# Optimization experiments

Measured on AMD Instinct MI355X. Metric: run time of the kernel, lower is better.

The kernel has to match this reference:

```python
import jax, jax.numpy as jnp
import numpy as np

IN_SIZE, R = 80, 5
D = 256  # hidden size used throughout
OUT = IN_SIZE * R  # 400


def gru_cell(x, h, Wih, Whh, bih, bhh):
    # torch.nn.GRUCell semantics
    gi = x @ Wih.T + bih
    gh = h @ Whh.T + bhh
    ir, iz, in_ = jnp.split(gi, 3, axis=-1)
    hr, hz, hn = jnp.split(gh, 3, axis=-1)
    r = jax.nn.sigmoid(ir + hr)
    z = jax.nn.sigmoid(iz + hz)
    n = jnp.tanh(in_ + r * hn)
    return (1.0 - z) * n + z * h


def setup_inputs() -> dict:
    key = jax.random.key(0)
    ks = jax.random.split(key, 32)
    s = 0.05
    inp = {
        'encoder_outputs': jax.random.normal(ks[0], (128, 512, D), jnp.float32),
        'inputs': jax.random.normal(ks[1], (128, 1000, IN_SIZE), jnp.float32),
        # Prenet: Linear(400,256), Linear(256,128)
        'W1': jax.random.normal(ks[2], (256, OUT)) * s, 'b1': jnp.zeros((256,)),
        'W2': jax.random.normal(ks[3], (128, 256)) * s, 'b2': jnp.zeros((128,)),
        # attn GRUCell(384 -> 256)
        'Wih_a': jax.random.normal(ks[4], (3 * D, 128 + D)) * s,
        'Whh_a': jax.random.normal(ks[5], (3 * D, D)) * s,
        'bih_a': jnp.zeros((3 * D,)), 'bhh_a': jnp.zeros((3 * D,)),
        # Bahdanau attention: query_layer (no bias) and v: Linear(256,1,no bias)
        'Wq': jax.random.normal(ks[6], (D, D)) * s,
        'v': jax.random.normal(ks[7], (D,)) * s,
        # memory_layer Linear(256,256,no bias)
        'Wm': jax.random.normal(ks[8], (D, D)) * s,
        # pre_rnn_dec_proj Linear(512,256)
        'Wp': jax.random.normal(ks[9], (D, 2 * D)) * s, 'bp': jnp.zeros((D,)),
        # two decoder GRUCells(256 -> 256)
        'Wih_d1': jax.random.normal(ks[10], (3 * D, D)) * s,
        'Whh_d1': jax.random.normal(ks[11], (3 * D, D)) * s,
        'bih_d1': jnp.zeros((3 * D,)), 'bhh_d1': jnp.zeros((3 * D,)),
        'Wih_d2': jax.random.normal(ks[12], (3 * D, D)) * s,
        'Whh_d2': jax.random.normal(ks[13], (3 * D, D)) * s,
        'bih_d2': jnp.zeros((3 * D,)), 'bhh_d2': jnp.zeros((3 * D,)),
        # mel projection Linear(256, 400)
        'Wmel': jax.random.normal(ks[14], (OUT, D)) * s, 'bmel': jnp.zeros((OUT,)),
    }
    return inp


def reference(encoder_outputs, inputs, W1, b1, W2, b2,
              Wih_a, Whh_a, bih_a, bhh_a, Wq, v, Wm, Wp, bp,
              Wih_d1, Whh_d1, bih_d1, bhh_d1,
              Wih_d2, Whh_d2, bih_d2, bhh_d2, Wmel, bmel):
    B = encoder_outputs.shape[0]
    processed_mem = encoder_outputs @ Wm.T               # (B, T_enc, D)
    # teacher forcing: (B, T_mel, in_size) -> (T_dec, B, in_size*r)
    x = inputs.reshape(B, inputs.shape[1] // R, -1).transpose(1, 0, 2)
    # decoder input at step t is frame t-1 (zeros at t=0)
    x_shift = jnp.concatenate([jnp.zeros_like(x[:1]), x[:-1]], axis=0)

    def step(carry, x_t):
        attn_h, h1, h2, ctx = carry
        # prenet (dropout disabled: eval-mode reference)
        pre = jax.nn.relu(x_t @ W1.T + b1)
        pre = jax.nn.relu(pre @ W2.T + b2)                # (B, 128)
        cell_in = jnp.concatenate([pre, ctx], axis=-1)    # (B, 384)
        attn_h = gru_cell(cell_in, attn_h, Wih_a, Whh_a, bih_a, bhh_a)
        q = attn_h @ Wq.T                                 # (B, D)
        logits = jnp.tanh(q[:, None, :] + processed_mem) @ v  # (B, T_enc)
        align = jax.nn.softmax(logits, axis=-1)
        ctx = jnp.einsum('bt,btd->bd', align, encoder_outputs)
        dec_in = jnp.concatenate([attn_h, ctx], axis=-1) @ Wp.T + bp
        h1 = gru_cell(dec_in, h1, Wih_d1, Whh_d1, bih_d1, bhh_d1)
        dec_in = h1 + dec_in
        h2 = gru_cell(dec_in, h2, Wih_d2, Whh_d2, bih_d2, bhh_d2)
        dec_in = h2 + dec_in
        out = dec_in @ Wmel.T + bmel                      # (B, 400)
        return (attn_h, h1, h2, ctx), (out, align)

    z = jnp.zeros((B, D), encoder_outputs.dtype)
    init = (z, z, z, z)
    _, (outs, aligns) = jax.lax.scan(step, init, x_shift)
    outputs = outs.transpose(1, 0, 2)       # (B, T_dec, 400)
    alignments = aligns.transpose(1, 0, 2)  # (B, T_dec, T_enc)
    return outputs, alignments
```

## Files before the change

### kernel.cpp

```cpp
#include <hip/hip_runtime.h>

typedef _Float16 h2f __attribute__((ext_vector_type(2)));

#define LOG2E 1.44269504088896f

__device__ __forceinline__ float fexp2(float x){ return __builtin_amdgcn_exp2f(x); }
__device__ __forceinline__ float frcp (float x){ return __builtin_amdgcn_rcpf(x); }
__device__ __forceinline__ float sigm (float x){ return frcp(1.f + fexp2(-LOG2E*x)); }
__device__ __forceinline__ float tanhf2(float x){
  x = fminf(15.f, fmaxf(-15.f, x));
  float e = fexp2(2.f*LOG2E*x);
  return (e-1.f)*frcp(e+1.f);
}
__device__ __forceinline__ unsigned pkh2(float a, float b){
  h2f h; h.x = (_Float16)a; h.y = (_Float16)b;
  return __builtin_bit_cast(unsigned, h);
}

#if __has_builtin(__builtin_amdgcn_fdot2)
__device__ __forceinline__ float dot2(unsigned a, unsigned b, float c){
  return __builtin_amdgcn_fdot2(__builtin_bit_cast(h2f,a), __builtin_bit_cast(h2f,b), c, false);
}
#else
__device__ __forceinline__ float dot2(unsigned a, unsigned b, float c){
  h2f ha=__builtin_bit_cast(h2f,a), hb=__builtin_bit_cast(h2f,b);
  return c + (float)ha.x*(float)hb.x + (float)ha.y*(float)hb.y;
}
#endif

__device__ __forceinline__ void dot8_2(uint4 w, uint4 x, float& a0, float& a1){
  a0 = dot2(w.x, x.x, a0); a1 = dot2(w.y, x.y, a1);
  a0 = dot2(w.z, x.z, a0); a1 = dot2(w.w, x.w, a1);
}

template<int N, int K8>
__device__ __forceinline__ float mv(const uint4* __restrict__ W, const uint4* __restrict__ xs, int n){
  float a0 = 0.f, a1 = 0.f;
  #pragma unroll 4
  for (int k8 = 0; k8 < K8; ++k8)
    dot8_2(W[k8*N + n], xs[k8], a0, a1);
  return a0 + a1;
}

template<int N, int K8, int C>
__device__ __forceinline__ float mvc(const uint4* __restrict__ W, const uint4* __restrict__ xs, int n){
  float a0 = 0.f, a1 = 0.f;
  int k8 = 0;
  #pragma unroll 1
  for (; k8 + C <= K8; k8 += C){
    uint4 w[C];
    #pragma unroll
    for (int i = 0; i < C; ++i) w[i] = W[(size_t)(k8+i)*N + n];
    #pragma unroll
    for (int i = 0; i < C; ++i) dot8_2(w[i], xs[k8+i], a0, a1);
  }
  if constexpr (K8 % C){
    constexpr int R = K8 % C;
    uint4 w[R];
    #pragma unroll
    for (int i = 0; i < R; ++i) w[i] = W[(size_t)(k8+i)*N + n];
    #pragma unroll
    for (int i = 0; i < R; ++i) dot8_2(w[i], xs[k8+i], a0, a1);
  }
  return a0 + a1;
}

static constexpr size_t OFF_W1   = 0;
static constexpr size_t OFF_W2   = 204800;
static constexpr size_t OFF_WIHA = 270336;
static constexpr size_t OFF_WHHA = 860160;
static constexpr size_t OFF_WQ   = 1253376;
static constexpr size_t OFF_WP   = 1384448;
static constexpr size_t OFF_WD1I = 1646592;
static constexpr size_t OFF_WD1H = 2039808;
static constexpr size_t OFF_WD2I = 2433024;
static constexpr size_t OFF_WD2H = 2826240;
static constexpr size_t OFF_WMEL = 3219456;
static constexpr size_t OFF_WM   = 3424256;
static constexpr size_t OFF_TPM  = 3555328;
static constexpr size_t OFF_ENCH = 37109760;

__global__ void pack_w(const float* __restrict__ src, uint4* __restrict__ dst, int N, int K8){
  int idx = blockIdx.x*blockDim.x + threadIdx.x;
  if (idx >= N*K8) return;
  int n = idx % N, k8 = idx / N;
  const float* s = src + (size_t)n*(K8*8) + k8*8;
  dst[idx] = make_uint4(pkh2(s[0],s[1]), pkh2(s[2],s[3]), pkh2(s[4],s[5]), pkh2(s[6],s[7]));
}

__global__ void conv_enc(const float* __restrict__ enc, unsigned* __restrict__ encH){
  size_t i = blockIdx.x*(size_t)blockDim.x + threadIdx.x;
  if (i >= (size_t)128*512*128) return;
  const float2 f = *(const float2*)(enc + 2*i);
  encH[i] = pkh2(f.x, f.y);
}

__global__ __launch_bounds__(1024) void pm_kernel(const float* __restrict__ enc,
    const uint4* __restrict__ Wmp, unsigned* __restrict__ tpm)
{
  int b = blockIdx.y, tc = blockIdx.x;
  int tid = threadIdx.x;
  __shared__ __align__(16) unsigned s_e[4][128];
  if (tid < 512){
    int r = tid >> 7, d2 = tid & 127;
    const float2 f = *(const float2*)(enc + ((size_t)b*512 + tc*4 + r)*256 + 2*d2);
    s_e[r][d2] = pkh2(f.x, f.y);
  }
  __syncthreads();
  int d = tid & 255, r = tid >> 8;
  float acc = mv<256,32>(Wmp, (const uint4*)s_e[r], d);
  float tq = tanhf2(acc);
  float hi = __shfl_down(tq, 1);
  if ((d & 1) == 0)
    tpm[(size_t)b*65536 + (size_t)(d>>1)*512 + (tc*4 + r)] = pkh2(tq, hi);
}

__global__ __launch_bounds__(256) void prenet_kernel(
    const float* __restrict__ inputs,
    const float* __restrict__ b1, const float* __restrict__ b2,
    const uint4* __restrict__ W1p, const uint4* __restrict__ W2p,
    float* __restrict__ out)
{
  int t = blockIdx.x, b = blockIdx.y;
  int tid = threadIdx.x;
  __shared__ __align__(16) unsigned s_x[200];
  __shared__ __align__(16) unsigned s_p1[128];
  __shared__ float s_a[256];
  if (tid < 200){
    unsigned xv = 0u;
    if (t > 0){
      const float2 f = *(const float2*)(inputs + (size_t)b*80000 + (size_t)(t-1)*400 + 2*tid);
      xv = pkh2(f.x, f.y);
    }
    s_x[tid] = xv;
  }
  __syncthreads();
  float a = fmaxf(mv<256,50>(W1p, (const uint4*)s_x, tid) + b1[tid], 0.f);
  s_a[tid] = a;
  __syncthreads();
  if (tid < 128) s_p1[tid] = pkh2(s_a[2*tid], s_a[2*tid+1]);
  __syncthreads();
  if (tid < 128){
    float p = fmaxf(mv<128,32>(W2p, (const uint4*)s_p1, tid) + b2[tid], 0.f);
    float pN = __shfl_down(p, 1);
    if (!(tid & 1)){
      unsigned* dst = (unsigned*)(out + (size_t)10240000 + ((size_t)b*200 + t)*512);
      dst[tid>>1] = pkh2(p, pN);
    }
  }
}

__global__ __launch_bounds__(512) void mel_kernel(
    const float* __restrict__ bmel, const uint4* __restrict__ Wmelp,
    float* __restrict__ out)
{
  int t = blockIdx.x, b = blockIdx.y;
  int tid = threadIdx.x;
  __shared__ __align__(16) unsigned s_d[128];
  float* po = out + ((size_t)b*200 + t)*400;
  if (tid < 128) s_d[tid] = ((const unsigned*)po)[tid];
  __syncthreads();
  if (tid < 400){
    float r = mvc<400,32,8>(Wmelp, (const uint4*)s_d, tid) + bmel[tid];
    __builtin_nontemporal_store(r, &po[tid]);
  }
}

__global__ __launch_bounds__(1024, 1) void decoder(
   const float* __restrict__ biha, const float* __restrict__ bhha,
   const float* __restrict__ vvec, const float* __restrict__ bp,
   const float* __restrict__ bd1i, const float* __restrict__ bd1h,
   const float* __restrict__ bd2i, const float* __restrict__ bd2h,
   const uint4* __restrict__ Wihap, const uint4* __restrict__ Whhap,
   const uint4* __restrict__ Wqp, const uint4* __restrict__ Wpp,
   const uint4* __restrict__ Wd1ip, const uint4* __restrict__ Wd1hp,
   const uint4* __restrict__ Wd2ip, const uint4* __restrict__ Wd2hp,
   const unsigned* __restrict__ tpm, const unsigned* __restrict__ encH,
   float* __restrict__ out)
{
  const int tid = threadIdx.x;
  const int b = blockIdx.x;

  __shared__ __align__(16) unsigned s_cin2[192];
  __shared__ __align__(16) unsigned s_cat2[256];
  __shared__ __align__(16) unsigned s_di2[128];
  __shared__ __align__(16) unsigned s_h12[128];
  __shared__ __align__(16) unsigned s_h22[128];
  __shared__ float  s_gha[768], s_gh1[768], s_gh2[768];
  __shared__ float  s_g[768];
  __shared__ float  s_ahf[256], s_h1f[256], s_h2f[256];
  __shared__ float  s_dif[256];
  __shared__ float4 s_tv[128];
  __shared__ float  s_lp[2][512];
  __shared__ float2 s_cp[8][128];
  __shared__ float  s_mvp[4][256];
  __shared__ float  s_align[512];
  __shared__ float  s_red[16];

  if (tid < 192) s_cin2[tid] = 0u;
  if (tid < 256){ s_cat2[tid]=0u; s_ahf[tid]=0.f; s_h1f[tid]=0.f; s_h2f[tid]=0.f; }
  if (tid < 128){ s_h12[tid]=0u; s_h22[tid]=0u;
                  s_tv[tid].z = vvec[2*tid]; s_tv[tid].w = vvec[2*tid+1]; }
  __syncthreads();

  const unsigned* tpmB = tpm  + (size_t)b*65536;
  const unsigned* encB = encH + (size_t)b*65536;
  float* outMel = out + (size_t)b*200*400;
  float* outAl  = out + (size_t)10240000 + (size_t)b*200*512;

  for (int t = 0; t < 200; ++t){
    if (tid < 768){
      s_gha[tid] = mvc<768,32,8>(Whhap, (const uint4*)s_cat2, tid) + bhha[tid];
    } else if (tid < 960){
      int r = tid - 768;
      s_gh2[r] = mvc<768,32,8>(Wd2hp, (const uint4*)s_h22, r) + bd2h[r];
    } else {
      s_cin2[tid-960] = ((const unsigned*)(outAl + (size_t)t*512))[tid-960];
    }
    __syncthreads();
    if (tid < 768){
      s_gh1[tid] = mvc<768,32,8>(Wd1hp, (const uint4*)s_h12, tid) + bd1h[tid];
    } else {
      int r = 192 + tid - 768;
      s_gh2[r] = mvc<768,32,8>(Wd2hp, (const uint4*)s_h22, r) + bd2h[r];
    }
    __syncthreads();
    if (tid < 768){
      float gi = mvc<768,48,8>(Wihap, (const uint4*)s_cin2, tid) + biha[tid];
      s_g[tid] = (tid < 512) ? sigm(gi + s_gha[tid]) : gi;
    } else {
      int r = 448 + tid - 768;
      s_gh2[r] = mvc<768,32,8>(Wd2hp, (const uint4*)s_h22, r) + bd2h[r];
    }
    __syncthreads();
    if (tid < 256){
      float rr = s_g[tid], z = s_g[256+tid];
      float nv = tanhf2(s_g[512+tid] + rr*s_gha[512+tid]);
      float h  = nv + z*(s_ahf[tid] - nv);
      s_ahf[tid] = h;
      float hN = __shfl_down(h, 1);
      if (!(tid&1)) s_cat2[tid>>1] = pkh2(h, hN);
    } else if (tid < 320){
      int r = 704 + tid - 256;
      s_gh2[r] = mvc<768,32,8>(Wd2hp, (const uint4*)s_h22, r) + bd2h[r];
    }
    __syncthreads();
    if (tid < 512){
      int n = tid & 255, p = tid >> 8;
      s_mvp[p][n] = mvc<256,16,8>(Wqp + (size_t)p*16*256, (const uint4*)s_cat2 + p*16, n);
    }
    __syncthreads();
    if (tid < 256){
      float q = s_mvp[0][tid] + s_mvp[1][tid];
      ((float*)&s_tv[tid>>1])[tid&1] = tanhf2(q);
    }
    __syncthreads();
    {
      int tt = tid & 511, dh = tid >> 9;
      const unsigned* tp = tpmB + tt + (size_t)dh*32768;
      float acc = 0.f;
      #pragma unroll 1
      for (int c = 0; c < 64; c += 16){
        unsigned tw[16];
        #pragma unroll
        for (int i = 0; i < 16; ++i) tw[i] = __builtin_nontemporal_load(&tp[(size_t)(c+i)*512]);
        #pragma unroll
        for (int i = 0; i < 16; ++i){
          h2f ta = __builtin_bit_cast(h2f, tw[i]);
          float4 tv = s_tv[dh*64 + c + i];
          float ta0 = (float)ta.x, ta1 = (float)ta.y;
          acc += tv.z*(ta0+tv.x)*frcp(1.f+ta0*tv.x)
               + tv.w*(ta1+tv.y)*frcp(1.f+ta1*tv.y);
        }
      }
      s_lp[dh][tt] = acc;
    }
    __syncthreads();
    float ee = 0.f;
    if (tid < 512){
      float lg = s_lp[0][tid] + s_lp[1][tid];
      ee = fexp2(LOG2E*lg);
      float s = ee;
      #pragma unroll
      for (int off = 32; off >= 1; off >>= 1) s += __shfl_xor(s, off);
      if ((tid & 63) == 0) s_red[tid>>6] = s;
    }
    __syncthreads();
    if (tid < 512){
      float S = (s_red[0]+s_red[1])+(s_red[2]+s_red[3])
              + (s_red[4]+s_red[5])+(s_red[6]+s_red[7]);
      float a = ee * frcp(S);
      s_align[tid] = a;
      __builtin_nontemporal_store(a, &outAl[(size_t)t*512 + tid]);
    }
    __syncthreads();
    {
      int d2 = tid & 127, tc = tid >> 7;
      const unsigned* eb = encB + d2 + (size_t)tc*8192;
      float ax = 0.f, ay = 0.f;
      #pragma unroll 1
      for (int c = 0; c < 64; c += 16){
        unsigned ew[16];
        #pragma unroll
        for (int i = 0; i < 16; ++i) ew[i] = __builtin_nontemporal_load(&eb[(size_t)(c+i)*128]);
        #pragma unroll
        for (int i = 0; i < 16; ++i){
          float a = s_align[tc*64 + c + i];
          h2f e2 = __builtin_bit_cast(h2f, ew[i]);
          ax += a*(float)e2.x; ay += a*(float)e2.y;
        }
      }
      s_cp[tc][d2] = make_float2(ax, ay);
    }
    __syncthreads();
    if (tid < 256){
      const float* cp = (const float*)s_cp;
      float c = 0.f;
      #pragma unroll
      for (int k = 0; k < 8; ++k) c += cp[k*256 + tid];
      float cN = __shfl_down(c, 1);
      if (!(tid&1)){ unsigned pk = pkh2(c, cN); s_cin2[64+(tid>>1)] = pk; s_cat2[128+(tid>>1)] = pk; }
    }
    __syncthreads();
    {
      int n = tid & 255, p = tid >> 8;
      s_mvp[p][n] = mvc<256,16,8>(Wpp + (size_t)p*16*256, (const uint4*)s_cat2 + p*16, n);
    }
    __syncthreads();
    if (tid < 256){
      float di = s_mvp[0][tid]+s_mvp[1][tid]+s_mvp[2][tid]+s_mvp[3][tid] + bp[tid];
      s_dif[tid] = di;
      float dN = __shfl_down(di, 1);
      if (!(tid&1)) s_di2[tid>>1] = pkh2(di, dN);
    }
    __syncthreads();
    if (tid < 768){
      float gi = mvc<768,32,8>(Wd1ip, (const uint4*)s_di2, tid) + bd1i[tid];
      s_g[tid] = (tid < 512) ? sigm(gi + s_gh1[tid]) : gi;
    }
    __syncthreads();
    if (tid < 256){
      float rr = s_g[tid], z = s_g[256+tid];
      float nv = tanhf2(s_g[512+tid] + rr*s_gh1[512+tid]);
      float h  = nv + z*(s_h1f[tid] - nv);
      s_h1f[tid] = h;
      float di = s_dif[tid] + h; s_dif[tid] = di;
      float hN = __shfl_down(h, 1), dN = __shfl_down(di, 1);
      if (!(tid&1)){ s_h12[tid>>1] = pkh2(h, hN); s_di2[tid>>1] = pkh2(di, dN); }
    }
    __syncthreads();
    if (tid < 768){
      float gi = mvc<768,32,8>(Wd2ip, (const uint4*)s_di2, tid) + bd2i[tid];
      s_g[tid] = (tid < 512) ? sigm(gi + s_gh2[tid]) : gi;
    }
    __syncthreads();
    if (tid < 256){
      float rr = s_g[tid], z = s_g[256+tid];
      float nv = tanhf2(s_g[512+tid] + rr*s_gh2[512+tid]);
      float h  = nv + z*(s_h2f[tid] - nv);
      s_h2f[tid] = h;
      float di = s_dif[tid] + h;
      float hN = __shfl_down(h, 1), dN = __shfl_down(di, 1);
      if (!(tid&1)){
        unsigned dpk = pkh2(di, dN);
        s_h22[tid>>1] = pkh2(h, hN);
        s_di2[tid>>1] = dpk;
        ((unsigned*)(outMel + (size_t)t*400))[tid>>1] = dpk;
      }
    }
    __syncthreads();
  }
}

extern "C" void kernel_launch(void* const* d_in, const int* in_sizes, int n_in,
                              void* d_out, int out_size, void* d_ws, size_t ws_size,
                              hipStream_t stream){
  (void)in_sizes; (void)n_in; (void)out_size; (void)ws_size;
  const float* enc    = (const float*)d_in[0];
  const float* inputs = (const float*)d_in[1];
  const float* W1 = (const float*)d_in[2];   const float* b1 = (const float*)d_in[3];
  const float* W2 = (const float*)d_in[4];   const float* b2 = (const float*)d_in[5];
  const float* Wiha = (const float*)d_in[6]; const float* Whha = (const float*)d_in[7];
  const float* biha = (const float*)d_in[8]; const float* bhha = (const float*)d_in[9];
  const float* Wq = (const float*)d_in[10];  const float* v  = (const float*)d_in[11];
  const float* Wm = (const float*)d_in[12];
  const float* Wp = (const float*)d_in[13];  const float* bp = (const float*)d_in[14];
  const float* Wd1i = (const float*)d_in[15]; const float* Wd1h = (const float*)d_in[16];
  const float* bd1i = (const float*)d_in[17]; const float* bd1h = (const float*)d_in[18];
  const float* Wd2i = (const float*)d_in[19]; const float* Wd2h = (const float*)d_in[20];
  const float* bd2i = (const float*)d_in[21]; const float* bd2h = (const float*)d_in[22];
  const float* Wmel = (const float*)d_in[23]; const float* bmel = (const float*)d_in[24];

  char* ws = (char*)d_ws;
  uint4* W1p   = (uint4*)(ws + OFF_W1);
  uint4* W2p   = (uint4*)(ws + OFF_W2);
  uint4* Wihap = (uint4*)(ws + OFF_WIHA);
  uint4* Whhap = (uint4*)(ws + OFF_WHHA);
  uint4* Wqp   = (uint4*)(ws + OFF_WQ);
  uint4* Wpp   = (uint4*)(ws + OFF_WP);
  uint4* Wd1ip = (uint4*)(ws + OFF_WD1I);
  uint4* Wd1hp = (uint4*)(ws + OFF_WD1H);
  uint4* Wd2ip = (uint4*)(ws + OFF_WD2I);
  uint4* Wd2hp = (uint4*)(ws + OFF_WD2H);
  uint4* Wmelp = (uint4*)(ws + OFF_WMEL);
  uint4* Wmp   = (uint4*)(ws + OFF_WM);
  unsigned* tpm  = (unsigned*)(ws + OFF_TPM);
  unsigned* encH = (unsigned*)(ws + OFF_ENCH);

  auto P = [&](const float* s, uint4* dst, int N, int K){
    int k8 = K/8, tot = N*k8;
    pack_w<<<(tot+255)/256, 256, 0, stream>>>(s, dst, N, k8);
  };
  P(W1, W1p, 256, 400);   P(W2, W2p, 128, 256);
  P(Wiha, Wihap, 768, 384); P(Whha, Whhap, 768, 256);
  P(Wq, Wqp, 256, 256);   P(Wm, Wmp, 256, 256);
  P(Wp, Wpp, 256, 512);
  P(Wd1i, Wd1ip, 768, 256); P(Wd1h, Wd1hp, 768, 256);
  P(Wd2i, Wd2ip, 768, 256); P(Wd2h, Wd2hp, 768, 256);
  P(Wmel, Wmelp, 400, 256);

  conv_enc<<<32768, 256, 0, stream>>>(enc, encH);
  pm_kernel<<<dim3(128,128), 1024, 0, stream>>>(enc, Wmp, tpm);
  prenet_kernel<<<dim3(200,128), 256, 0, stream>>>(inputs, b1, b2, W1p, W2p, (float*)d_out);

  decoder<<<128, 1024, 0, stream>>>(
      biha, bhha, v, bp, bd1i, bd1h, bd2i, bd2h,
      Wihap, Whhap, Wqp, Wpp, Wd1ip, Wd1hp, Wd2ip, Wd2hp,
      tpm, encH, (float*)d_out);

  mel_kernel<<<dim3(200,128), 512, 0, stream>>>(bmel, Wmelp, (float*)d_out);
}
```

Baseline: 8.842 ms.

## Process two batch elements per decoder block to reuse weight loads

Measured after the change: 12.90 ms. 45.9% more time.

```diff
diff --git a/kernel.cpp b/kernel.cpp
--- a/kernel.cpp
+++ b/kernel.cpp
@@ -45,24 +45,34 @@
 template<int N, int K8, int C>
 __device__ __forceinline__ float mvc(const uint4* __restrict__ W, const uint4* __restrict__ xs, int n){
   float a0 = 0.f, a1 = 0.f;
-  int k8 = 0;
   #pragma unroll 1
-  for (; k8 + C <= K8; k8 += C){
+  for (int k8 = 0; k8 + C <= K8; k8 += C){
     uint4 w[C];
     #pragma unroll
     for (int i = 0; i < C; ++i) w[i] = W[(size_t)(k8+i)*N + n];
     #pragma unroll
     for (int i = 0; i < C; ++i) dot8_2(w[i], xs[k8+i], a0, a1);
   }
-  if constexpr (K8 % C){
-    constexpr int R = K8 % C;
-    uint4 w[R];
+  return a0 + a1;
+}
+
+template<int N, int K8, int C>
+__device__ __forceinline__ void mvc2(const uint4* __restrict__ W,
+    const uint4* __restrict__ xs0, const uint4* __restrict__ xs1, int n,
+    float& o0, float& o1){
+  float a0=0.f, b0=0.f, a1=0.f, b1=0.f;
+  #pragma unroll 1
+  for (int k8 = 0; k8 < K8; k8 += C){
+    uint4 w[C];
     #pragma unroll
-    for (int i = 0; i < R; ++i) w[i] = W[(size_t)(k8+i)*N + n];
+    for (int i = 0; i < C; ++i) w[i] = W[(size_t)(k8+i)*N + n];
     #pragma unroll
-    for (int i = 0; i < R; ++i) dot8_2(w[i], xs[k8+i], a0, a1);
-  }
-  return a0 + a1;
+    for (int i = 0; i < C; ++i){
+      dot8_2(w[i], xs0[k8+i], a0, b0);
+      dot8_2(w[i], xs1[k8+i], a1, b1);
+    }
+  }
+  o0 = a0 + b0; o1 = a1 + b1;
 }
 
 static constexpr size_t OFF_W1   = 0;
@@ -111,8 +121,10 @@
   float acc = mv<256,32>(Wmp, (const uint4*)s_e[r], d);
   float tq = tanhf2(acc);
   float hi = __shfl_down(tq, 1);
-  if ((d & 1) == 0)
-    tpm[(size_t)b*65536 + (size_t)(d>>1)*512 + (tc*4 + r)] = pkh2(tq, hi);
+  if ((d & 1) == 0){
+    int t = tc*4 + r;
+    tpm[ (((size_t)b*32 + (d>>3))*512 + t)*4 + ((d>>1)&3) ] = pkh2(tq, hi);
+  }
 }
 
 __global__ __launch_bounds__(256) void prenet_kernel(
@@ -179,193 +191,240 @@
    float* __restrict__ out)
 {
   const int tid = threadIdx.x;
-  const int b = blockIdx.x;
-
-  __shared__ __align__(16) unsigned s_cin2[192];
-  __shared__ __align__(16) unsigned s_cat2[256];
-  __shared__ __align__(16) unsigned s_di2[128];
-  __shared__ __align__(16) unsigned s_h12[128];
-  __shared__ __align__(16) unsigned s_h22[128];
-  __shared__ float  s_gha[768], s_gh1[768], s_gh2[768];
-  __shared__ float  s_g[768];
-  __shared__ float  s_ahf[256], s_h1f[256], s_h2f[256];
-  __shared__ float  s_dif[256];
-  __shared__ float4 s_tv[128];
+  const int b0 = 2*blockIdx.x, b1v = b0 + 1;
+
+  __shared__ __align__(16) unsigned s_cin2[2][192];
+  __shared__ __align__(16) unsigned s_cat2[2][256];
+  __shared__ __align__(16) unsigned s_di2[2][128];
+  __shared__ __align__(16) unsigned s_h12[2][128];
+  __shared__ __align__(16) unsigned s_h22[2][128];
+  __shared__ float  s_gha[2][768], s_gh1[2][768], s_gh2[2][768];
+  __shared__ float  s_g[2][768];
+  __shared__ float  s_ahf[2][256], s_h1f[2][256], s_h2f[2][256];
+  __shared__ float  s_dif[2][256];
+  __shared__ float4 s_tv[2][128];
   __shared__ float  s_lp[2][512];
-  __shared__ float2 s_cp[8][128];
-  __shared__ float  s_mvp[4][256];
-  __shared__ float  s_align[512];
-  __shared__ float  s_red[16];
-
-  if (tid < 192) s_cin2[tid] = 0u;
-  if (tid < 256){ s_cat2[tid]=0u; s_ahf[tid]=0.f; s_h1f[tid]=0.f; s_h2f[tid]=0.f; }
-  if (tid < 128){ s_h12[tid]=0u; s_h22[tid]=0u;
-                  s_tv[tid].z = vvec[2*tid]; s_tv[tid].w = vvec[2*tid+1]; }
-  __syncthreads();
-
-  const unsigned* tpmB = tpm  + (size_t)b*65536;
-  const unsigned* encB = encH + (size_t)b*65536;
-  float* outMel = out + (size_t)b*200*400;
-  float* outAl  = out + (size_t)10240000 + (size_t)b*200*512;
+  __shared__ float2 s_cp[2][16][32][4];
+  __shared__ float  s_mvp[2][4][256];
+  __shared__ float  s_align[2][512];
+  __shared__ float  s_red[2][8];
+
+  if (tid < 384){ int be=tid/192, i=tid%192; s_cin2[be][i] = 0u; }
+  if (tid < 512){ int be=tid>>8, i=tid&255;
+    s_cat2[be][i]=0u; s_ahf[be][i]=0.f; s_h1f[be][i]=0.f; s_h2f[be][i]=0.f; }
+  if (tid < 256){ int be=tid>>7, i=tid&127;
+    s_h12[be][i]=0u; s_h22[be][i]=0u;
+    s_tv[be][i].z = vvec[2*i]; s_tv[be][i].w = vvec[2*i+1]; }
+  __syncthreads();
+
+  const unsigned* encB[2] = { encH + (size_t)b0*65536, encH + (size_t)b1v*65536 };
+  const uint4*    tpm4[2] = { (const uint4*)tpm + (size_t)b0*16384,
+                              (const uint4*)tpm + (size_t)b1v*16384 };
+  float* outMel[2] = { out + (size_t)b0*80000, out + (size_t)b1v*80000 };
+  float* outAl [2] = { out + 10240000ull + (size_t)b0*102400,
+                       out + 10240000ull + (size_t)b1v*102400 };
+
+  const uint4* cin4[2] = { (const uint4*)s_cin2[0], (const uint4*)s_cin2[1] };
+  const uint4* cat4[2] = { (const uint4*)s_cat2[0], (const uint4*)s_cat2[1] };
+  const uint4* di4 [2] = { (const uint4*)s_di2[0],  (const uint4*)s_di2[1]  };
+  const uint4* h14 [2] = { (const uint4*)s_h12[0],  (const uint4*)s_h12[1]  };
+  const uint4* h24 [2] = { (const uint4*)s_h22[0],  (const uint4*)s_h22[1]  };
 
   for (int t = 0; t < 200; ++t){
     if (tid < 768){
-      s_gha[tid] = mvc<768,32,8>(Whhap, (const uint4*)s_cat2, tid) + bhha[tid];
+      float o0,o1; mvc2<768,32,8>(Whhap, cat4[0], cat4[1], tid, o0, o1);
+      s_gha[0][tid] = o0 + bhha[tid]; s_gha[1][tid] = o1 + bhha[tid];
     } else if (tid < 960){
       int r = tid - 768;
-      s_gh2[r] = mvc<768,32,8>(Wd2hp, (const uint4*)s_h22, r) + bd2h[r];
+      float o0,o1; mvc2<768,32,8>(Wd2hp, h24[0], h24[1], r, o0, o1);
+      s_gh2[0][r] = o0 + bd2h[r]; s_gh2[1][r] = o1 + bd2h[r];
     } else {
-      s_cin2[tid-960] = ((const unsigned*)(outAl + (size_t)t*512))[tid-960];
+      int j = tid - 960;
+      s_cin2[0][j] = ((const unsigned*)(outAl[0] + (size_t)t*512))[j];
+      s_cin2[1][j] = ((const unsigned*)(outAl[1] + (size_t)t*512))[j];
     }
     __syncthreads();
     if (tid < 768){
-      s_gh1[tid] = mvc<768,32,8>(Wd1hp, (const uint4*)s_h12, tid) + bd1h[tid];
+      float o0,o1; mvc2<768,32,8>(Wd1hp, h14[0], h14[1], tid, o0, o1);
+      s_gh1[0][tid] = o0 + bd1h[tid]; s_gh1[1][tid] = o1 + bd1h[tid];
     } else {
       int r = 192 + tid - 768;
-      s_gh2[r] = mvc<768,32,8>(Wd2hp, (const uint4*)s_h22, r) + bd2h[r];
+      float o0,o1; mvc2<768,32,8>(Wd2hp, h24[0], h24[1], r, o0, o1);
+      s_gh2[0][r] = o0 + bd2h[r]; s_gh2[1][r] = o1 + bd2h[r];
     }
     __syncthreads();
     if (tid < 768){
-      float gi = mvc<768,48,8>(Wihap, (const uint4*)s_cin2, tid) + biha[tid];
-      s_g[tid] = (tid < 512) ? sigm(gi + s_gha[tid]) : gi;
+      float o0,o1; mvc2<768,48,8>(Wihap, cin4[0], cin4[1], tid, o0, o1);
+      o0 += biha[tid]; o1 += biha[tid];
+      if (tid < 512){ s_g[0][tid] = sigm(o0 + s_gha[0][tid]); s_g[1][tid] = sigm(o1 + s_gha[1][tid]); }
+      else          { s_g[0][tid] = o0;                        s_g[1][tid] = o1; }
     } else {
       int r = 448 + tid - 768;
-      s_gh2[r] = mvc<768,32,8>(Wd2hp, (const uint4*)s_h22, r) + bd2h[r];
-    }
-    __syncthreads();
-    if (tid < 256){
-      float rr = s_g[tid], z = s_g[256+tid];
-      float nv = tanhf2(s_g[512+tid] + rr*s_gha[512+tid]);
-      float h  = nv + z*(s_ahf[tid] - nv);
-      s_ahf[tid] = h;
+      float o0,o1; mvc2<768,32,8>(Wd2hp, h24[0], h24[1], r, o0, o1);
+      s_gh2[0][r] = o0 + bd2h[r]; s_gh2[1][r] = o1 + bd2h[r];
+    }
+    __syncthreads();
+    if (tid < 512){
+      int be = tid>>8, i = tid&255;
+      float rr = s_g[be][i], z = s_g[be][256+i];
+      float nv = tanhf2(s_g[be][512+i] + rr*s_gha[be][512+i]);
+      float h  = nv + z*(s_ahf[be][i] - nv);
+      s_ahf[be][i] = h;
       float hN = __shfl_down(h, 1);
-      if (!(tid&1)) s_cat2[tid>>1] = pkh2(h, hN);
-    } else if (tid < 320){
-      int r = 704 + tid - 256;
-      s_gh2[r] = mvc<768,32,8>(Wd2hp, (const uint4*)s_h22, r) + bd2h[r];
-    }
-    __syncthreads();
-    if (tid < 512){
-      int n = tid & 255, p = tid >> 8;
-      s_mvp[p][n] = mvc<256,16,8>(Wqp + (size_t)p*16*256, (const uint4*)s_cat2 + p*16, n);
-    }
-    __syncthreads();
-    if (tid < 256){
-      float q = s_mvp[0][tid] + s_mvp[1][tid];
-      ((float*)&s_tv[tid>>1])[tid&1] = tanhf2(q);
-    }
-    __syncthreads();
-    {
-      int tt = tid & 511, dh = tid >> 9;
-      const unsigned* tp = tpmB + tt + (size_t)dh*32768;
+      if (!(i&1)) s_cat2[be][i>>1] = pkh2(h, hN);
+    } else if (tid < 576){
+      int r = 704 + tid - 512;
+      float o0,o1; mvc2<768,32,8>(Wd2hp, h24[0], h24[1], r, o0, o1);
+      s_gh2[0][r] = o0 + bd2h[r]; s_gh2[1][r] = o1 + bd2h[r];
+    }
+    __syncthreads();
+    {
+      int n = tid & 255, p = (tid>>8)&3;
+      float o0,o1; mvc2<256,8,8>(Wqp + (size_t)p*8*256, cat4[0]+p*8, cat4[1]+p*8, n, o0, o1);
+      s_mvp[0][p][n] = o0; s_mvp[1][p][n] = o1;
+    }
+    __syncthreads();
+    if (tid < 512){
+      int be = tid>>8, i = tid&255;
+      float q = s_mvp[be][0][i]+s_mvp[be][1][i]+s_mvp[be][2][i]+s_mvp[be][3][i];
+      ((float*)&s_tv[be][i>>1])[i&1] = tanhf2(q);
+    }
+    __syncthreads();
+    {
+      int be = tid>>9, tt = tid&511;
+      const uint4* tp = tpm4[be] + tt;
       float acc = 0.f;
       #pragma unroll 1
-      for (int c = 0; c < 64; c += 16){
-        unsigned tw[16];
+      for (int g = 0; g < 32; g += 8){
+        uint4 T[8];
         #pragma unroll
-        for (int i = 0; i < 16; ++i) tw[i] = __builtin_nontemporal_load(&tp[(size_t)(c+i)*512]);
+        for (int i = 0; i < 8; ++i) T[i] = tp[(size_t)(g+i)*512];
         #pragma unroll
-        for (int i = 0; i < 16; ++i){
-          h2f ta = __builtin_bit_cast(h2f, tw[i]);
-          float4 tv = s_tv[dh*64 + c + i];
-          float ta0 = (float)ta.x, ta1 = (float)ta.y;
-          acc += tv.z*(ta0+tv.x)*frcp(1.f+ta0*tv.x)
-               + tv.w*(ta1+tv.y)*frcp(1.f+ta1*tv.y);
+        for (int i = 0; i < 8; ++i){
+          #pragma unroll
+          for (int j = 0; j < 4; ++j){
+            unsigned u = ((const unsigned*)&T[i])[j];
+            h2f ta = __builtin_bit_cast(h2f, u);
+            float4 tv = s_tv[be][(g+i)*4 + j];
+            float ta0 = (float)ta.x, ta1 = (float)ta.y;
+            float n0 = ta0 + tv.x, n1 = ta1 + tv.y;
+            float d0 = fmaf(ta0, tv.x, 1.f), d1 = fmaf(ta1, tv.y, 1.f);
+            float r  = frcp(d0*d1);
+            acc = fmaf(fmaf(tv.w*n1, d0, (tv.z*n0)*d1), r, acc);
+          }
         }
       }
-      s_lp[dh][tt] = acc;
+      s_lp[be][tt] = acc;
     }
     __syncthreads();
     float ee = 0.f;
-    if (tid < 512){
-      float lg = s_lp[0][tid] + s_lp[1][tid];
+    {
+      int be = tid>>9, tt = tid&511;
+      float lg = s_lp[be][tt];
       ee = fexp2(LOG2E*lg);
       float s = ee;
       #pragma unroll
       for (int off = 32; off >= 1; off >>= 1) s += __shfl_xor(s, off);
-      if ((tid & 63) == 0) s_red[tid>>6] = s;
-    }
-    __syncthreads();
-    if (tid < 512){
-      float S = (s_red[0]+s_red[1])+(s_red[2]+s_red[3])
-              + (s_red[4]+s_red[5])+(s_red[6]+s_red[7]);
+      if ((tid & 63) == 0) s_red[be][tt>>6] = s;
+    }
+    __syncthreads();
+    {
+      int be = tid>>9, tt = tid&511;
+      float S = (s_red[be][0]+s_red[be][1])+(s_red[be][2]+s_red[be][3])
+              + (s_red[be][4]+s_red[be][5])+(s_red[be][6]+s_red[be][7]);
       float a = ee * frcp(S);
-      s_align[tid] = a;
-      __builtin_nontemporal_store(a, &outAl[(size_t)t*512 + tid]);
-    }
-    __syncthreads();
-    {
-      int d2 = tid & 127, tc = tid >> 7;
-      const unsigned* eb = encB + d2 + (size_t)tc*8192;
-      float ax = 0.f, ay = 0.f;
+      s_align[be][tt] = a;
+      __builtin_nontemporal_store(a, &outAl[be][(size_t)t*512 + tt]);
+    }
+    __syncthreads();
+    {
+      int be = tid>>9, ts = (tid>>5)&15, g = tid&31;
+      const uint4* e4 = (const uint4*)encB[be] + (size_t)(ts*32)*32 + g;
+      float2 c0={0,0}, c1={0,0}, c2={0,0}, c3={0,0};
       #pragma unroll 1
-      for (int c = 0; c < 64; c += 16){
-        unsigned ew[16];
+      for (int u = 0; u < 32; u += 8){
+        uint4 E[8];
         #pragma unroll
-        for (int i = 0; i < 16; ++i) ew[i] = __builtin_nontemporal_load(&eb[(size_t)(c+i)*128]);
+        for (int i = 0; i < 8; ++i) E[i] = e4[(size_t)(u+i)*32];
         #pragma unroll
-        for (int i = 0; i < 16; ++i){
-          float a = s_align[tc*64 + c + i];
-          h2f e2 = __builtin_bit_cast(h2f, ew[i]);
-          ax += a*(float)e2.x; ay += a*(float)e2.y;
+        for (int i = 0; i < 8; ++i){
+          float a = s_align[be][ts*32 + u + i];
+          h2f e0 = __builtin_bit_cast(h2f, E[i].x);
+          h2f e1 = __builtin_bit_cast(h2f, E[i].y);
+          h2f e2 = __builtin_bit_cast(h2f, E[i].z);
+          h2f e3 = __builtin_bit_cast(h2f, E[i].w);
+          c0.x += a*(float)e0.x; c0.y += a*(float)e0.y;
+          c1.x += a*(float)e1.x; c1.y += a*(float)e1.y;
+          c2.x += a*(float)e2.x; c2.y += a*(float)e2.y;
+          c3.x += a*(float)e3.x; c3.y += a*(float)e3.y;
         }
       }
-      s_cp[tc][d2] = make_float2(ax, ay);
-    }
-    __syncthreads();
-    if (tid < 256){
-      const float* cp = (const float*)s_cp;
+      s_cp[be][ts][g][0] = c0; s_cp[be][ts][g][1] = c1;
+      s_cp[be][ts][g][2] = c2; s_cp[be][ts][g][3] = c3;
+    }
+    __syncthreads();
+    if (tid < 512){
+      int be = tid>>8, d = tid&255;
+      int d2 = d>>1, g = d2>>2, j = d2&3, comp = d&1;
+      const float* base = (const float*)s_cp + ((size_t)be*16*32*4*2) + (size_t)g*8 + j*2 + comp;
       float c = 0.f;
       #pragma unroll
-      for (int k = 0; k < 8; ++k) c += cp[k*256 + tid];
+      for (int ts = 0; ts < 16; ++ts) c += base[(size_t)ts*32*4*2];
       float cN = __shfl_down(c, 1);
-      if (!(tid&1)){ unsigned pk = pkh2(c, cN); s_cin2[64+(tid>>1)] = pk; s_cat2[128+(tid>>1)] = pk; }
-    }
-    __syncthreads();
-    {
-      int n = tid & 255, p = tid >> 8;
-      s_mvp[p][n] = mvc<256,16,8>(Wpp + (size_t)p*16*256, (const uint4*)s_cat2 + p*16, n);
-    }
-    __syncthreads();
-    if (tid < 256){
-      float di = s_mvp[0][tid]+s_mvp[1][tid]+s_mvp[2][tid]+s_mvp[3][tid] + bp[tid];
-      s_dif[tid] = di;
+      if (!(d&1)){ unsigned pk = pkh2(c, cN); s_cin2[be][64+d2] = pk; s_cat2[be][128+d2] = pk; }
+    }
+    __syncthreads();
+    {
+      int n = tid & 255, p = (tid>>8)&3;
+      float o0,o1; mvc2<256,16,8>(Wpp + (size_t)p*16*256, cat4[0]+p*16, cat4[1]+p*16, n, o0, o1);
+      s_mvp[0][p][n] = o0; s_mvp[1][p][n] = o1;
+    }
+    __syncthreads();
+    if (tid < 512){
+      int be = tid>>8, i = tid&255;
+      float di = s_mvp[be][0][i]+s_mvp[be][1][i]+s_mvp[be][2][i]+s_mvp[be][3][i] + bp[i];
+      s_dif[be][i] = di;
       float dN = __shfl_down(di, 1);
-      if (!(tid&1)) s_di2[tid>>1] = pkh2(di, dN);
+      if (!(i&1)) s_di2[be][i>>1] = pkh2(di, dN);
     }
     __syncthreads();
     if (tid < 768){
-      float gi = mvc<768,32,8>(Wd1ip, (const uint4*)s_di2, tid) + bd1i[tid];
-      s_g[tid] = (tid < 512) ? sigm(gi + s_gh1[tid]) : gi;
-    }
-    __syncthreads();
-    if (tid < 256){
-      float rr = s_g[tid], z = s_g[256+tid];
-      float nv = tanhf2(s_g[512+tid] + rr*s_gh1[512+tid]);
-      float h  = nv + z*(s_h1f[tid] - nv);
-      s_h1f[tid] = h;
-      float di = s_dif[tid] + h; s_dif[tid] = di;
+      float o0,o1; mvc2<768,32,8>(Wd1ip, di4[0], di4[1], tid, o0, o1);
+      o0 += bd1i[tid]; o1 += bd1i[tid];
+      if (tid < 512){ s_g[0][tid] = sigm(o0 + s_gh1[0][tid]); s_g[1][tid] = sigm(o1 + s_gh1[1][tid]); }
+      else          { s_g[0][tid] = o0;                        s_g[1][tid] = o1; }
+    }
+    __syncthreads();
+    if (tid < 512){
+      int be = tid>>8, i = tid&255;
+      float rr = s_g[be][i], z = s_g[be][256+i];
+      float nv = tanhf2(s_g[be][512+i] + rr*s_gh1[be][512+i]);
+      float h  = nv + z*(s_h1f[be][i] - nv);
+      s_h1f[be][i] = h;
+      float di = s_dif[be][i] + h; s_dif[be][i] = di;
       float hN = __shfl_down(h, 1), dN = __shfl_down(di, 1);
-      if (!(tid&1)){ s_h12[tid>>1] = pkh2(h, hN); s_di2[tid>>1] = pkh2(di, dN); }
+      if (!(i&1)){ s_h12[be][i>>1] = pkh2(h, hN); s_di2[be][i>>1] = pkh2(di, dN); }
     }
     __syncthreads();
     if (tid < 768){
-      float gi = mvc<768,32,8>(Wd2ip, (const uint4*)s_di2, tid) + bd2i[tid];
-      s_g[tid] = (tid < 512) ? sigm(gi + s_gh2[tid]) : gi;
-    }
-    __syncthreads();
-    if (tid < 256){
-      float rr = s_g[tid], z = s_g[256+tid];
-      float nv = tanhf2(s_g[512+tid] + rr*s_gh2[512+tid]);
-      float h  = nv + z*(s_h2f[tid] - nv);
-      s_h2f[tid] = h;
-      float di = s_dif[tid] + h;
+      float o0,o1; mvc2<768,32,8>(Wd2ip, di4[0], di4[1], tid, o0, o1);
+      o0 += bd2i[tid]; o1 += bd2i[tid];
+      if (tid < 512){ s_g[0][tid] = sigm(o0 + s_gh2[0][tid]); s_g[1][tid] = sigm(o1 + s_gh2[1][tid]); }
+      else          { s_g[0][tid] = o0;                        s_g[1][tid] = o1; }
+    }
+    __syncthreads();
+    if (tid < 512){
+      int be = tid>>8, i = tid&255;
+      float rr = s_g[be][i], z = s_g[be][256+i];
+      float nv = tanhf2(s_g[be][512+i] + rr*s_gh2[be][512+i]);
+      float h  = nv + z*(s_h2f[be][i] - nv);
+      s_h2f[be][i] = h;
+      float di = s_dif[be][i] + h;
       float hN = __shfl_down(h, 1), dN = __shfl_down(di, 1);
-      if (!(tid&1)){
+      if (!(i&1)){
         unsigned dpk = pkh2(di, dN);
-        s_h22[tid>>1] = pkh2(h, hN);
-        s_di2[tid>>1] = dpk;
-        ((unsigned*)(outMel + (size_t)t*400))[tid>>1] = dpk;
+        s_h22[be][i>>1] = pkh2(h, hN);
+        ((unsigned*)(outMel[be] + (size_t)t*400))[i>>1] = dpk;
       }
     }
     __syncthreads();
@@ -423,7 +482,7 @@
   pm_kernel<<<dim3(128,128), 1024, 0, stream>>>(enc, Wmp, tpm);
   prenet_kernel<<<dim3(200,128), 256, 0, stream>>>(inputs, b1, b2, W1p, W2p, (float*)d_out);
 
-  decoder<<<128, 1024, 0, stream>>>(
+  decoder<<<64, 1024, 0, stream>>>(
       biha, bhha, v, bp, bd1i, bd1h, bd2i, bd2h,
       Wihap, Whhap, Wqp, Wpp, Wd1ip, Wd1hp, Wd2ip, Wd2hp,
       tpm, encH, (float*)d_out);
```
